# Kernel optimization log

Measured on AMD Instinct MI355X. Metric: run time of the kernel, lower is better.

## Reference

```python
import jax, jax.numpy as jnp
import numpy as np

N_NODES = 100000
N_EDGES = 3200000
IN_DIM = 256
HID = 64
OUT_DIM = 1


def gcn_conv(x, W, b, src, dst, n):
    # PyG GCNConv: h = x @ W; add self loops; sym-normalize; aggregate; + b
    h = x @ W  # [N, F]
    # degrees include self loops (edge_weight = 1), computed on target nodes
    ones = jnp.ones(src.shape[0], dtype=x.dtype)
    deg = jax.ops.segment_sum(ones, dst, num_segments=n) + 1.0  # +1 for self loop
    dinv = jax.lax.rsqrt(deg)
    norm = dinv[src] * dinv[dst]  # [E]
    msg = h[src] * norm[:, None]  # gather + scale
    out = jax.ops.segment_sum(msg, dst, num_segments=n)
    # self-loop contribution: norm_ii = dinv[i]^2
    out = out + h * (dinv * dinv)[:, None]
    return out + b


def setup_inputs() -> dict:
    key = jax.random.key(0)
    ks = jax.random.split(key, 6)
    x = jax.random.normal(ks[0], (N_NODES, IN_DIM), dtype=jnp.float32)
    edge_index = jax.random.randint(ks[1], (2, N_EDGES), 0, N_NODES, dtype=jnp.int64)
    W1 = jax.random.normal(ks[2], (IN_DIM, HID), dtype=jnp.float32) / np.sqrt(IN_DIM)
    b1 = jnp.zeros((HID,), dtype=jnp.float32)
    W2 = jax.random.normal(ks[3], (HID, HID), dtype=jnp.float32) / np.sqrt(HID)
    b2 = jnp.zeros((HID,), dtype=jnp.float32)
    Wf = jax.random.normal(ks[4], (HID, OUT_DIM), dtype=jnp.float32) / np.sqrt(HID)
    bf = jnp.zeros((OUT_DIM,), dtype=jnp.float32)
    return {"x": x, "edge_index": edge_index, "W1": W1, "b1": b1,
            "W2": W2, "b2": b2, "Wf": Wf, "bf": bf}


def reference(x, edge_index, W1, b1, W2, b2, Wf, bf):
    src, dst = edge_index[0], edge_index[1]
    n = x.shape[0]
    h = jax.nn.relu(gcn_conv(x, W1, b1, src, dst, n))
    h = jax.nn.relu(gcn_conv(h, W2, b2, src, dst, n))
    g = jnp.mean(h, axis=0)  # [HID] graph readout
    return jax.nn.sigmoid(g @ Wf + bf)  # [OUT_DIM]
```

## Files before the change

### kernel.cpp

```cpp
#include <hip/hip_runtime.h>


typedef unsigned int u32;
typedef unsigned short u16;
typedef unsigned char u8;
typedef short s16x8 __attribute__((ext_vector_type(8)));
typedef __bf16 bf16x8 __attribute__((ext_vector_type(8)));
typedef float f32x4 __attribute__((ext_vector_type(4)));

constexpr int HID  = 64;
constexpr int SH   = 7;
constexpr int BK   = 128;
constexpr int BPAD = 1024;
constexpr int CH   = 4096;
constexpr int SLOT = 5120;
constexpr int NBLK2 = 4096;

static __device__ __forceinline__ u8 f2fp8(float f) {
    int p = __builtin_amdgcn_cvt_pk_fp8_f32(f, f, 0, false);
    return (u8)(p & 0xFF);
}
static __device__ __forceinline__ float fp82f(u8 v) {
    return __builtin_amdgcn_cvt_f32_fp8((int)v, 0);
}
static __device__ __forceinline__ u16 f2bf(float f) {
    u32 u = __float_as_uint(f);
    return (u16)((u + 0x7FFFu + ((u >> 16) & 1u)) >> 16);
}

__global__ void init_bcur_kernel(int* __restrict__ bcur, int B) {
    int b = blockIdx.x * 256 + threadIdx.x;
    if (b < B) bcur[b] = b * SLOT;
}

__global__ __launch_bounds__(256) void partition_kernel(const int* __restrict__ src,
                                                        const int* __restrict__ dst,
                                                        int* __restrict__ bcur,
                                                        u32* __restrict__ ep, int ne) {
    __shared__ int hcnt[BPAD];
    __shared__ int hoff[BPAD];
    __shared__ int gbase[BPAD];
    __shared__ u32 stage[CH];
    __shared__ int ssc[256];
    const int t = threadIdx.x;
    const int base = blockIdx.x * CH;
    const int cnt = min(CH, ne - base);
    for (int i = t; i < BPAD; i += 256) hcnt[i] = 0;
    __syncthreads();

    int myr[CH / 256];
    #pragma unroll
    for (int k = 0; k < CH / 256; ++k) {
        int i = t + k * 256;
        if (i < cnt) myr[k] = atomicAdd(&hcnt[dst[base + i] >> SH], 1);
    }
    __syncthreads();
    {
        int c0 = hcnt[t*4], c1 = hcnt[t*4+1], c2 = hcnt[t*4+2], c3 = hcnt[t*4+3];
        int tsum = c0 + c1 + c2 + c3;
        ssc[t] = tsum; __syncthreads();
        int run = tsum;
        for (int off = 1; off < 256; off <<= 1) {
            int v = (t >= off) ? ssc[t - off] : 0;
            __syncthreads();
            run += v; ssc[t] = run;
            __syncthreads();
        }
        int ex = run - tsum;
        hoff[t*4] = ex; ex += c0;
        hoff[t*4+1] = ex; ex += c1;
        hoff[t*4+2] = ex; ex += c2;
        hoff[t*4+3] = ex;
    }
    __syncthreads();
    for (int b = t; b < BPAD; b += 256) {
        int c = hcnt[b];
        if (c) gbase[b] = atomicAdd(&bcur[b], c);
    }
    #pragma unroll
    for (int k = 0; k < CH / 256; ++k) {
        int i = t + k * 256;
        if (i < cnt) {
            int s = src[base + i], d = dst[base + i];
            stage[hoff[d >> SH] + myr[k]] = ((u32)(d & (BK - 1)) << 20) | (u32)s;
        }
    }
    __syncthreads();
    for (int i = t; i < cnt; i += 256) {
        u32 v = stage[i];
        int lo = 0;
        #pragma unroll
        for (int s = 512; s; s >>= 1) {
            int m = lo + s;
            if (m < BPAD && hoff[m] <= i) lo = m;
        }
        ep[gbase[lo] + (i - hoff[lo])] = v;
    }
}

__global__ __launch_bounds__(256) void bucket_sort_kernel(const u32* __restrict__ ep,
                                                          const int* __restrict__ bcur,
                                                          int* __restrict__ eidx,
                                                          int* __restrict__ rowend,
                                                          float* __restrict__ dinv, int n) {
    __shared__ int cnt[BK];
    __shared__ int sc[BK];
    __shared__ int cur[BK];
    const int t = threadIdx.x, b = blockIdx.x;
    const int beg = b * SLOT, end = bcur[b];
    if (t < BK) cnt[t] = 0;
    __syncthreads();
    for (int p = beg + t; p < end; p += 256) atomicAdd(&cnt[ep[p] >> 20], 1);
    __syncthreads();
    if (t < BK) sc[t] = cnt[t];
    __syncthreads();
    for (int o = 1; o < BK; o <<= 1) {
        int v = 0;
        if (t < BK && t >= o) v = sc[t - o];
        __syncthreads();
        if (t < BK) sc[t] += v;
        __syncthreads();
    }
    if (t < BK) {
        int node = b * BK + t;
        if (node < n) {
            rowend[node] = beg + sc[t];
            dinv[node] = rsqrtf((float)cnt[t] + 1.0f);
        }
        cur[t] = beg + sc[t] - cnt[t];
    }
    __syncthreads();
    for (int p = beg + t; p < end; p += 256) {
        u32 v = ep[p];
        int r = atomicAdd(&cur[v >> 20], 1);
        eidx[r] = (int)(v & 0xFFFFFu);
    }
}

template <int K>
__global__ void pack_w_kernel(const float* __restrict__ W, u16* __restrict__ wpack) {
    int i = blockIdx.x * 256 + threadIdx.x;
    if (i >= K * 64) return;
    int e = i & 7, lane = (i >> 3) & 63, nt = (i >> 9) & 3, kk = i >> 11;
    int k = kk * 32 + (lane >> 4) * 8 + e;
    int c = nt * 16 + (lane & 15);
    wpack[i] = f2bf(W[k * HID + c]);
}

template <int K, typename TIn>
__global__ __launch_bounds__(256) void mfma_gemm_kernel(const TIn* __restrict__ A,
                                                        const u16* __restrict__ wpack,
                                                        const float* __restrict__ dinv,
                                                        u8* __restrict__ out8, int n) {
    const int t = threadIdx.x;
    const int lane = t & 63;
    const int wid = t >> 6;
    const int r16 = lane & 15;
    const int kgrp = lane >> 4;
    const int ntiles = (n + 15) >> 4;
    for (int tile = blockIdx.x * 4 + wid; tile < ntiles; tile += gridDim.x * 4) {
        const int row0 = tile * 16;
        const int arow = row0 + r16;
        f32x4 acc[4] = {f32x4{0,0,0,0}, f32x4{0,0,0,0}, f32x4{0,0,0,0}, f32x4{0,0,0,0}};
        #pragma unroll
        for (int kk = 0; kk < K / 32; ++kk) {
            s16x8 abits;
            if constexpr (sizeof(TIn) == 4) {
                const float* Af = (const float*)A;
                if (arow < n) {
                    const float4* p0 = (const float4*)(Af + (size_t)arow * K + kk * 32 + kgrp * 8);
                    float4 v0 = p0[0], v1 = p0[1];
                    abits[0] = (short)f2bf(v0.x); abits[1] = (short)f2bf(v0.y);
                    abits[2] = (short)f2bf(v0.z); abits[3] = (short)f2bf(v0.w);
                    abits[4] = (short)f2bf(v1.x); abits[5] = (short)f2bf(v1.y);
                    abits[6] = (short)f2bf(v1.z); abits[7] = (short)f2bf(v1.w);
                } else {
                    #pragma unroll
                    for (int j = 0; j < 8; ++j) abits[j] = 0;
                }
            } else {
                const u8* Ab = (const u8*)A;
                u32 w0 = 0, w1 = 0;
                if (arow < n) {
                    const u32* p0 = (const u32*)(Ab + (size_t)arow * K + kk * 32 + kgrp * 8);
                    w0 = p0[0]; w1 = p0[1];
                }
                abits[0] = (short)f2bf(__builtin_amdgcn_cvt_f32_fp8((int)w0, 0));
                abits[1] = (short)f2bf(__builtin_amdgcn_cvt_f32_fp8((int)w0, 1));
                abits[2] = (short)f2bf(__builtin_amdgcn_cvt_f32_fp8((int)w0, 2));
                abits[3] = (short)f2bf(__builtin_amdgcn_cvt_f32_fp8((int)w0, 3));
                abits[4] = (short)f2bf(__builtin_amdgcn_cvt_f32_fp8((int)w1, 0));
                abits[5] = (short)f2bf(__builtin_amdgcn_cvt_f32_fp8((int)w1, 1));
                abits[6] = (short)f2bf(__builtin_amdgcn_cvt_f32_fp8((int)w1, 2));
                abits[7] = (short)f2bf(__builtin_amdgcn_cvt_f32_fp8((int)w1, 3));
            }
            bf16x8 afrag = __builtin_bit_cast(bf16x8, abits);
            const u16* wp = wpack + ((size_t)(kk * 4) * 64 + lane) * 8;
            #pragma unroll
            for (int nt = 0; nt < 4; ++nt) {
                bf16x8 bfrag = *(const bf16x8*)(wp + (size_t)nt * 64 * 8);
                acc[nt] = __builtin_amdgcn_mfma_f32_16x16x32_bf16(afrag, bfrag, acc[nt], 0, 0, 0);
            }
        }
        #pragma unroll
        for (int reg = 0; reg < 4; ++reg) {
            int r = row0 + kgrp * 4 + reg;
            if (r < n) {
                float dv = dinv[r];
                #pragma unroll
                for (int nt = 0; nt < 4; ++nt)
                    out8[(size_t)r * HID + nt * 16 + r16] = f2fp8(acc[nt][reg] * dv);
            }
        }
    }
}

#define CVT4(acc0, acc1, acc2, acc3, wv) \
    acc0 += __builtin_amdgcn_cvt_f32_fp8((int)(wv), 0); \
    acc1 += __builtin_amdgcn_cvt_f32_fp8((int)(wv), 1); \
    acc2 += __builtin_amdgcn_cvt_f32_fp8((int)(wv), 2); \
    acc3 += __builtin_amdgcn_cvt_f32_fp8((int)(wv), 3);

__global__ __launch_bounds__(256) void agg_csr_kernel(const u8* __restrict__ hp,
                                                      const int* __restrict__ eidx,
                                                      const int* __restrict__ rowend,
                                                      const float* __restrict__ dinv,
                                                      const float* __restrict__ bias,
                                                      u8* __restrict__ out, int n) {
    int w = (blockIdx.x * 256 + threadIdx.x) >> 6;
    int lane = threadIdx.x & 63;
    if (w >= n) return;
    const int g = lane >> 4, fb = lane & 15;
    int beg = (w & (BK - 1)) ? rowend[w - 1] : (w >> SH) * SLOT;
    int end = rowend[w];
    float a0 = 0.f, a1 = 0.f, a2 = 0.f, a3 = 0.f;
    int p = beg;
    for (; p + 16 <= end; p += 16) {
        int s0 = __builtin_nontemporal_load(eidx + p + g);
        int s1 = __builtin_nontemporal_load(eidx + p + 4 + g);
        int s2 = __builtin_nontemporal_load(eidx + p + 8 + g);
        int s3 = __builtin_nontemporal_load(eidx + p + 12 + g);
        u32 w0 = *(const u32*)(hp + (size_t)s0 * 64 + fb * 4);
        u32 w1 = *(const u32*)(hp + (size_t)s1 * 64 + fb * 4);
        u32 w2 = *(const u32*)(hp + (size_t)s2 * 64 + fb * 4);
        u32 w3 = *(const u32*)(hp + (size_t)s3 * 64 + fb * 4);
        CVT4(a0, a1, a2, a3, w0)
        CVT4(a0, a1, a2, a3, w1)
        CVT4(a0, a1, a2, a3, w2)
        CVT4(a0, a1, a2, a3, w3)
    }
    for (; p < end; p += 4) {
        int idx = p + g;
        bool valid = idx < end;
        int s = __builtin_nontemporal_load(eidx + (valid ? idx : beg));
        u32 wv = *(const u32*)(hp + (size_t)s * 64 + fb * 4);
        if (valid) { CVT4(a0, a1, a2, a3, wv) }
    }
    a0 += __shfl_xor(a0, 16); a0 += __shfl_xor(a0, 32);
    a1 += __shfl_xor(a1, 16); a1 += __shfl_xor(a1, 32);
    a2 += __shfl_xor(a2, 16); a2 += __shfl_xor(a2, 32);
    a3 += __shfl_xor(a3, 16); a3 += __shfl_xor(a3, 32);
    u32 sv = *(const u32*)(hp + (size_t)w * 64 + fb * 4);
    float dv = dinv[w];
    float v0 = fmaxf(dv * (a0 + __builtin_amdgcn_cvt_f32_fp8((int)sv, 0)) + bias[fb * 4 + 0], 0.f);
    float v1 = fmaxf(dv * (a1 + __builtin_amdgcn_cvt_f32_fp8((int)sv, 1)) + bias[fb * 4 + 1], 0.f);
    float v2 = fmaxf(dv * (a2 + __builtin_amdgcn_cvt_f32_fp8((int)sv, 2)) + bias[fb * 4 + 2], 0.f);
    float v3 = fmaxf(dv * (a3 + __builtin_amdgcn_cvt_f32_fp8((int)sv, 3)) + bias[fb * 4 + 3], 0.f);
    if (g == 0) {
        int r = __builtin_amdgcn_cvt_pk_fp8_f32(v0, v1, 0, false);
        r = __builtin_amdgcn_cvt_pk_fp8_f32(v2, v3, r, true);
        *(u32*)(out + (size_t)w * 64 + fb * 4) = (u32)r;
    }
}

__global__ __launch_bounds__(256) void agg_csr_reduce_kernel(const u8* __restrict__ hp,
                                                             const int* __restrict__ eidx,
                                                             const int* __restrict__ rowend,
                                                             const float* __restrict__ dinv,
                                                             const float* __restrict__ bias,
                                                             float* __restrict__ partials, int n) {
    __shared__ float sred[256];
    int t = threadIdx.x, lane = t & 63;
    const int g = lane >> 4, fb = lane & 15;
    int wid = (blockIdx.x * 256 + t) >> 6;
    int wstride = gridDim.x * 4;
    float bl0 = bias[fb * 4 + 0], bl1 = bias[fb * 4 + 1];
    float bl2 = bias[fb * 4 + 2], bl3 = bias[fb * 4 + 3];
    float t0 = 0.f, t1 = 0.f, t2 = 0.f, t3 = 0.f;
    for (int w = wid; w < n; w += wstride) {
        int beg = (w & (BK - 1)) ? rowend[w - 1] : (w >> SH) * SLOT;
        int end = rowend[w];
        float a0 = 0.f, a1 = 0.f, a2 = 0.f, a3 = 0.f;
        int p = beg;
        for (; p + 16 <= end; p += 16) {
            int s0 = __builtin_nontemporal_load(eidx + p + g);
            int s1 = __builtin_nontemporal_load(eidx + p + 4 + g);
            int s2 = __builtin_nontemporal_load(eidx + p + 8 + g);
            int s3 = __builtin_nontemporal_load(eidx + p + 12 + g);
            u32 w0 = *(const u32*)(hp + (size_t)s0 * 64 + fb * 4);
            u32 w1 = *(const u32*)(hp + (size_t)s1 * 64 + fb * 4);
            u32 w2 = *(const u32*)(hp + (size_t)s2 * 64 + fb * 4);
            u32 w3 = *(const u32*)(hp + (size_t)s3 * 64 + fb * 4);
            CVT4(a0, a1, a2, a3, w0)
            CVT4(a0, a1, a2, a3, w1)
            CVT4(a0, a1, a2, a3, w2)
            CVT4(a0, a1, a2, a3, w3)
        }
        for (; p < end; p += 4) {
            int idx = p + g;
            bool valid = idx < end;
            int s = __builtin_nontemporal_load(eidx + (valid ? idx : beg));
            u32 wv = *(const u32*)(hp + (size_t)s * 64 + fb * 4);
            if (valid) { CVT4(a0, a1, a2, a3, wv) }
        }
        a0 += __shfl_xor(a0, 16); a0 += __shfl_xor(a0, 32);
        a1 += __shfl_xor(a1, 16); a1 += __shfl_xor(a1, 32);
        a2 += __shfl_xor(a2, 16); a2 += __shfl_xor(a2, 32);
        a3 += __shfl_xor(a3, 16); a3 += __shfl_xor(a3, 32);
        u32 sv = *(const u32*)(hp + (size_t)w * 64 + fb * 4);
        float dv = dinv[w];
        t0 += fmaxf(dv * (a0 + __builtin_amdgcn_cvt_f32_fp8((int)sv, 0)) + bl0, 0.f);
        t1 += fmaxf(dv * (a1 + __builtin_amdgcn_cvt_f32_fp8((int)sv, 1)) + bl1, 0.f);
        t2 += fmaxf(dv * (a2 + __builtin_amdgcn_cvt_f32_fp8((int)sv, 2)) + bl2, 0.f);
        t3 += fmaxf(dv * (a3 + __builtin_amdgcn_cvt_f32_fp8((int)sv, 3)) + bl3, 0.f);
    }
    int wv_ = t >> 6;
    if (g == 0) {
        sred[wv_ * 64 + fb * 4 + 0] = t0;
        sred[wv_ * 64 + fb * 4 + 1] = t1;
        sred[wv_ * 64 + fb * 4 + 2] = t2;
        sred[wv_ * 64 + fb * 4 + 3] = t3;
    }
    __syncthreads();
    if (t < 64) partials[blockIdx.x * 64 + t] = sred[t] + sred[t + 64] + sred[t + 128] + sred[t + 192];
}

__global__ __launch_bounds__(256) void gsum_stage_kernel(const float* __restrict__ parts, int nblk,
                                                         float* __restrict__ gsum) {
    __shared__ float sred[256];
    int t = threadIdx.x, col = t & 63;
    float a = 0.f;
    for (int bk = blockIdx.x * 4 + (t >> 6); bk < nblk; bk += gridDim.x * 4)
        a += parts[bk * 64 + col];
    sred[t] = a; __syncthreads();
    if (t < 64) atomicAdd(&gsum[t], sred[t] + sred[t + 64] + sred[t + 128] + sred[t + 192]);
}

__global__ void final_gsum_kernel(const float* __restrict__ gsum, const float* __restrict__ Wf,
                                  const float* __restrict__ bf_, float* __restrict__ out, float invn) {
    int lane = threadIdx.x;
    float v = gsum[lane] * invn * Wf[lane];
    #pragma unroll
    for (int off = 32; off; off >>= 1) v += __shfl_down(v, off);
    if (lane == 0) out[0] = 1.f / (1.f + expf(-(v + bf_[0])));
}

template <int K, typename TIn>
__global__ __launch_bounds__(256) void gemm_scale_kernel(const TIn* __restrict__ A,
                                                         const float* __restrict__ W,
                                                         const float* __restrict__ dinv,
                                                         u8* __restrict__ out8, int n) {
    __shared__ float xs[16][K];
    const int t = threadIdx.x;
    const int row0 = blockIdx.x * 16;
    if constexpr (sizeof(TIn) == 4) {
        const float* Af = (const float*)A;
        for (int i = t; i < 16 * K; i += 256) {
            int r = i / K;
            (&xs[0][0])[i] = (row0 + r < n) ? Af[(size_t)row0 * K + i] : 0.f;
        }
    } else {
        const u8* Ab = (const u8*)A;
        for (int i = t; i < 16 * K; i += 256) {
            int r = i / K;
            (&xs[0][0])[i] = (row0 + r < n) ? fp82f(Ab[(size_t)row0 * K + i]) : 0.f;
        }
    }
    __syncthreads();
    const int c = t & 63, rg = t >> 6;
    float acc[4] = {0.f, 0.f, 0.f, 0.f};
    #pragma unroll 4
    for (int k = 0; k < K; ++k) {
        float w = W[k * HID + c];
        #pragma unroll
        for (int j = 0; j < 4; ++j) acc[j] += xs[rg + 4 * j][k] * w;
    }
    #pragma unroll
    for (int j = 0; j < 4; ++j) {
        int r = row0 + rg + 4 * j;
        if (r < n) out8[(size_t)r * HID + c] = f2fp8(acc[j] * dinv[r]);
    }
}
__global__ void deg_f_kernel(const int* __restrict__ dst, float* __restrict__ deg, int ne) {
    int i = blockIdx.x * blockDim.x + threadIdx.x, st = gridDim.x * blockDim.x;
    for (; i < ne; i += st) atomicAdd(&deg[dst[i]], 1.0f);
}
__global__ void dinvf_kernel(float* __restrict__ deg, int n) {
    int i = blockIdx.x * blockDim.x + threadIdx.x;
    if (i < n) deg[i] = rsqrtf(deg[i] + 1.0f);
}
__global__ __launch_bounds__(256) void aggregate_atomic_kernel(const u8* __restrict__ hp,
        const int* __restrict__ src, const int* __restrict__ dst,
        const float* __restrict__ dinv, float* __restrict__ outf, int ne) {
    size_t tt = (size_t)blockIdx.x * 256 + threadIdx.x;
    int e = (int)(tt >> 6), f = (int)(tt & 63);
    if (e >= ne) return;
    int s = src[e], d = dst[e];
    atomicAdd(&outf[(size_t)d * HID + f], fp82f(hp[s * HID + f]) * dinv[d]);
}
__global__ void finalize1_fb_kernel(u8* __restrict__ hp, const float* __restrict__ agg,
                                    const float* __restrict__ dinv, const float* __restrict__ b, int n) {
    size_t i = (size_t)blockIdx.x * blockDim.x + threadIdx.x;
    if (i >= (size_t)n * HID) return;
    int node = (int)(i >> 6);
    float v = agg[i] + fp82f(hp[i]) * dinv[node] + b[i & 63];
    hp[i] = f2fp8(fmaxf(v, 0.f));
}
__global__ __launch_bounds__(256) void finalize2_fb_kernel(const u8* __restrict__ hp,
        const float* __restrict__ agg, const float* __restrict__ dinv,
        const float* __restrict__ b, float* __restrict__ gsum, int n) {
    __shared__ float sred[256];
    const int t = threadIdx.x, c = t & 63;
    const size_t total = (size_t)n * HID;
    const size_t stride = (size_t)gridDim.x * blockDim.x;
    float acc = 0.f;
    for (size_t i = (size_t)blockIdx.x * blockDim.x + t; i < total; i += stride) {
        int node = (int)(i >> 6);
        acc += fmaxf(agg[i] + fp82f(hp[i]) * dinv[node] + b[c], 0.f);
    }
    sred[t] = acc; __syncthreads();
    if (t < 64) atomicAdd(&gsum[c], sred[t] + sred[t + 64] + sred[t + 128] + sred[t + 192]);
}
__global__ void final_gsum_fb_kernel(const float* __restrict__ gsum, const float* __restrict__ Wf,
                                     const float* __restrict__ bf_, float* __restrict__ out, int n) {
    int lane = threadIdx.x;
    float v = (gsum[lane] / (float)n) * Wf[lane];
    #pragma unroll
    for (int off = 32; off; off >>= 1) v += __shfl_down(v, off);
    if (lane == 0) out[0] = 1.f / (1.f + expf(-(v + bf_[0])));
}

extern "C" void kernel_launch(void* const* d_in, const int* in_sizes, int n_in,
                              void* d_out, int out_size, void* d_ws, size_t ws_size,
                              hipStream_t stream) {
    const float* x  = (const float*)d_in[0];
    const int*   ei = (const int*)d_in[1];
    const float* W1 = (const float*)d_in[2];
    const float* b1 = (const float*)d_in[3];
    const float* W2 = (const float*)d_in[4];
    const float* b2 = (const float*)d_in[5];
    const float* Wf = (const float*)d_in[6];
    const float* bf_ = (const float*)d_in[7];
    float* out = (float*)d_out;

    const int n  = in_sizes[0] / 256;
    const int ne = in_sizes[1] / 2;
    const int* srcp = ei;
    const int* dstp = ei + ne;
    const int B = (n + BK - 1) / BK;

    char* p = (char*)d_ws;
    u32*   ep     = (u32*)p;   p += ((size_t)B * SLOT + 4096) * 4;
    int*   bcur   = (int*)p;   p += BPAD * 4;
    float* dinv   = (float*)p; p += (size_t)n * 4;
    int*   rowend = (int*)p;   p += (size_t)n * 4;
    float* gsum   = (float*)p; p += 64 * 4;
    int*   eidx   = (int*)p;   p += ((size_t)B * SLOT + 4096) * 4;
    float* parts  = (float*)p; p += (size_t)NBLK2 * 64 * 4;
    p = (char*)(((uintptr_t)p + 15) & ~(uintptr_t)15);
    u16*   wpack1 = (u16*)p;   p += 256 * 64 * 2;
    u16*   wpack2 = (u16*)p;   p += 64 * 64 * 2;
    u8*    hp     = (u8*)p;    p += (size_t)n * HID;
    u8*    h1     = (u8*)p;    p += (size_t)n * HID;
    size_t need = (size_t)(p - (char*)d_ws);

    bool slack_ok = ((size_t)ne / (size_t)B) <= (size_t)(SLOT - 1024);

    if (ws_size >= need && n <= (1 << 17) && slack_ok) {
        (void)hipMemsetAsync(gsum, 0, 64 * 4, stream);
        init_bcur_kernel<<<(B + 255) / 256, 256, 0, stream>>>(bcur, B);
        partition_kernel<<<(ne + CH - 1) / CH, 256, 0, stream>>>(srcp, dstp, bcur, ep, ne);
        bucket_sort_kernel<<<B, 256, 0, stream>>>(ep, bcur, eidx, rowend, dinv, n);
        pack_w_kernel<256><<<64, 256, 0, stream>>>(W1, wpack1);
        pack_w_kernel<64><<<16, 256, 0, stream>>>(W2, wpack2);

        const int ntiles = (n + 15) / 16;
        const int gblk = (ntiles + 3) / 4;
        mfma_gemm_kernel<256, float><<<gblk, 256, 0, stream>>>(x, wpack1, dinv, hp, n);
        agg_csr_kernel<<<(n + 3) / 4, 256, 0, stream>>>(hp, eidx, rowend, dinv, b1, h1, n);
        mfma_gemm_kernel<64, u8><<<gblk, 256, 0, stream>>>(h1, wpack2, dinv, hp, n);
        agg_csr_reduce_kernel<<<NBLK2, 256, 0, stream>>>(hp, eidx, rowend, dinv, b2, parts, n);
        gsum_stage_kernel<<<128, 256, 0, stream>>>(parts, NBLK2, gsum);
        final_gsum_kernel<<<1, 64, 0, stream>>>(gsum, Wf, bf_, out, 1.0f / (float)n);
    } else {
        char* q = (char*)d_ws;
        float* dinvF = (float*)q; q += (size_t)n * 4;
        float* gsumF = (float*)q; q += 64 * 4;
        u8*    hpF   = (u8*)q;   q += (size_t)n * HID;
        float* aggF  = (float*)q;

        (void)hipMemsetAsync(dinvF, 0, ((size_t)n + 64) * 4, stream);
        deg_f_kernel<<<2048, 256, 0, stream>>>(dstp, dinvF, ne);
        dinvf_kernel<<<(n + 255) / 256, 256, 0, stream>>>(dinvF, n);

        gemm_scale_kernel<256, float><<<(n + 15) / 16, 256, 0, stream>>>(x, W1, dinvF, hpF, n);
        (void)hipMemsetAsync(aggF, 0, (size_t)n * HID * 4, stream);
        aggregate_atomic_kernel<<<(int)(((size_t)ne * 64 + 255) / 256), 256, 0, stream>>>(hpF, srcp, dstp, dinvF, aggF, ne);
        finalize1_fb_kernel<<<(int)(((size_t)n * HID + 255) / 256), 256, 0, stream>>>(hpF, aggF, dinvF, b1, n);

        gemm_scale_kernel<64, u8><<<(n + 15) / 16, 256, 0, stream>>>(hpF, W2, dinvF, hpF, n);
        (void)hipMemsetAsync(aggF, 0, (size_t)n * HID * 4, stream);
        aggregate_atomic_kernel<<<(int)(((size_t)ne * 64 + 255) / 256), 256, 0, stream>>>(hpF, srcp, dstp, dinvF, aggF, ne);
        finalize2_fb_kernel<<<2048, 256, 0, stream>>>(hpF, aggF, dinvF, b2, gsumF, n);
        final_gsum_fb_kernel<<<1, 64, 0, stream>>>(gsumF, Wf, bf_, out, n);
    }
}
```

Before: 258.6 us.

## Fuse edge partitioning with layer-1 GEMM and defer dinv scaling to bucket sort

Merges the edge partition pass and the first-layer MFMA GEMM into one launch, with disjoint block ranges, so the compute-bound GEMM and the scatter-bound partition share the GPU at the same time. Because dinv is not yet known during the GEMM, the unscaled result is stored in fp8, and bucket_sort rescales each row by dinv in place. It also makes bcur a relative counter so one memset clears it and gsum together, and merges the two weight-pack kernels. The cost is an extra read-modify-write of hp and a second fp8 rounding step, which may change numerics slightly.

```diff
diff --git a/kernel.cpp b/kernel.cpp
--- a/kernel.cpp
+++ b/kernel.cpp
@@ -28,73 +28,132 @@
     return (u16)((u + 0x7FFFu + ((u >> 16) & 1u)) >> 16);
 }
 
-__global__ void init_bcur_kernel(int* __restrict__ bcur, int B) {
-    int b = blockIdx.x * 256 + threadIdx.x;
-    if (b < B) bcur[b] = b * SLOT;
-}
-
-__global__ __launch_bounds__(256) void partition_kernel(const int* __restrict__ src,
-                                                        const int* __restrict__ dst,
-                                                        int* __restrict__ bcur,
-                                                        u32* __restrict__ ep, int ne) {
+__global__ void pack_both_kernel(const float* __restrict__ W1, const float* __restrict__ W2,
+                                 u16* __restrict__ wpack1, u16* __restrict__ wpack2) {
+    int i = blockIdx.x * 256 + threadIdx.x;
+    if (i < 256 * 64) {
+        int e = i & 7, lane = (i >> 3) & 63, nt = (i >> 9) & 3, kk = i >> 11;
+        wpack1[i] = f2bf(W1[(kk * 32 + (lane >> 4) * 8 + e) * HID + nt * 16 + (lane & 15)]);
+    } else {
+        int j = i - 256 * 64;
+        if (j < 64 * 64) {
+            int e = j & 7, lane = (j >> 3) & 63, nt = (j >> 9) & 3, kk = j >> 11;
+            wpack2[j] = f2bf(W2[(kk * 32 + (lane >> 4) * 8 + e) * HID + nt * 16 + (lane & 15)]);
+        }
+    }
+}
+
+__global__ __launch_bounds__(256) void mega1_kernel(const int* __restrict__ src,
+                                                    const int* __restrict__ dst,
+                                                    int* __restrict__ bcur,
+                                                    u32* __restrict__ ep, int ne,
+                                                    const float* __restrict__ x,
+                                                    const u16* __restrict__ wpack1,
+                                                    u8* __restrict__ hp, int n,
+                                                    int PBLK, int GBLK) {
     __shared__ int hcnt[BPAD];
     __shared__ int hoff[BPAD];
     __shared__ int gbase[BPAD];
     __shared__ u32 stage[CH];
     __shared__ int ssc[256];
     const int t = threadIdx.x;
-    const int base = blockIdx.x * CH;
-    const int cnt = min(CH, ne - base);
-    for (int i = t; i < BPAD; i += 256) hcnt[i] = 0;
-    __syncthreads();
-
-    int myr[CH / 256];
-    #pragma unroll
-    for (int k = 0; k < CH / 256; ++k) {
-        int i = t + k * 256;
-        if (i < cnt) myr[k] = atomicAdd(&hcnt[dst[base + i] >> SH], 1);
-    }
-    __syncthreads();
-    {
-        int c0 = hcnt[t*4], c1 = hcnt[t*4+1], c2 = hcnt[t*4+2], c3 = hcnt[t*4+3];
-        int tsum = c0 + c1 + c2 + c3;
-        ssc[t] = tsum; __syncthreads();
-        int run = tsum;
-        for (int off = 1; off < 256; off <<= 1) {
-            int v = (t >= off) ? ssc[t - off] : 0;
-            __syncthreads();
-            run += v; ssc[t] = run;
-            __syncthreads();
-        }
-        int ex = run - tsum;
-        hoff[t*4] = ex; ex += c0;
-        hoff[t*4+1] = ex; ex += c1;
-        hoff[t*4+2] = ex; ex += c2;
-        hoff[t*4+3] = ex;
-    }
-    __syncthreads();
-    for (int b = t; b < BPAD; b += 256) {
-        int c = hcnt[b];
-        if (c) gbase[b] = atomicAdd(&bcur[b], c);
-    }
-    #pragma unroll
-    for (int k = 0; k < CH / 256; ++k) {
-        int i = t + k * 256;
-        if (i < cnt) {
-            int s = src[base + i], d = dst[base + i];
-            stage[hoff[d >> SH] + myr[k]] = ((u32)(d & (BK - 1)) << 20) | (u32)s;
-        }
-    }
-    __syncthreads();
-    for (int i = t; i < cnt; i += 256) {
-        u32 v = stage[i];
-        int lo = 0;
+
+    if ((int)blockIdx.x < PBLK) {
+        const int base = blockIdx.x * CH;
+        const int cnt = min(CH, ne - base);
+        for (int i = t; i < BPAD; i += 256) hcnt[i] = 0;
+        __syncthreads();
+        int myr[CH / 256];
         #pragma unroll
-        for (int s = 512; s; s >>= 1) {
-            int m = lo + s;
-            if (m < BPAD && hoff[m] <= i) lo = m;
-        }
-        ep[gbase[lo] + (i - hoff[lo])] = v;
+        for (int k = 0; k < CH / 256; ++k) {
+            int i = t + k * 256;
+            if (i < cnt) myr[k] = atomicAdd(&hcnt[dst[base + i] >> SH], 1);
+        }
+        __syncthreads();
+        {
+            int c0 = hcnt[t*4], c1 = hcnt[t*4+1], c2 = hcnt[t*4+2], c3 = hcnt[t*4+3];
+            int tsum = c0 + c1 + c2 + c3;
+            ssc[t] = tsum; __syncthreads();
+            int run = tsum;
+            for (int off = 1; off < 256; off <<= 1) {
+                int v = (t >= off) ? ssc[t - off] : 0;
+                __syncthreads();
+                run += v; ssc[t] = run;
+                __syncthreads();
+            }
+            int ex = run - tsum;
+            hoff[t*4] = ex; ex += c0;
+            hoff[t*4+1] = ex; ex += c1;
+            hoff[t*4+2] = ex; ex += c2;
+            hoff[t*4+3] = ex;
+        }
+        __syncthreads();
+        for (int b = t; b < BPAD; b += 256) {
+            int c = hcnt[b];
+            if (c) gbase[b] = b * SLOT + atomicAdd(&bcur[b], c);
+        }
+        #pragma unroll
+        for (int k = 0; k < CH / 256; ++k) {
+            int i = t + k * 256;
+            if (i < cnt) {
+                int s = src[base + i], d = dst[base + i];
+                stage[hoff[d >> SH] + myr[k]] = ((u32)(d & (BK - 1)) << 20) | (u32)s;
+            }
+        }
+        __syncthreads();
+        for (int i = t; i < cnt; i += 256) {
+            u32 v = stage[i];
+            int lo = 0;
+            #pragma unroll
+            for (int s = 512; s; s >>= 1) {
+                int m = lo + s;
+                if (m < BPAD && hoff[m] <= i) lo = m;
+            }
+            ep[gbase[lo] + (i - hoff[lo])] = v;
+        }
+    } else {
+        const int gbid = blockIdx.x - PBLK;
+        const int lane = t & 63;
+        const int wid = t >> 6;
+        const int r16 = lane & 15;
+        const int kgrp = lane >> 4;
+        const int ntiles = (n + 15) >> 4;
+        for (int tile = gbid * 4 + wid; tile < ntiles; tile += GBLK * 4) {
+            const int row0 = tile * 16;
+            const int arow = row0 + r16;
+            f32x4 acc[4] = {f32x4{0,0,0,0}, f32x4{0,0,0,0}, f32x4{0,0,0,0}, f32x4{0,0,0,0}};
+            #pragma unroll
+            for (int kk = 0; kk < 256 / 32; ++kk) {
+                s16x8 abits;
+                if (arow < n) {
+                    const float4* p0 = (const float4*)(x + (size_t)arow * 256 + kk * 32 + kgrp * 8);
+                    float4 v0 = p0[0], v1 = p0[1];
+                    abits[0] = (short)f2bf(v0.x); abits[1] = (short)f2bf(v0.y);
+                    abits[2] = (short)f2bf(v0.z); abits[3] = (short)f2bf(v0.w);
+                    abits[4] = (short)f2bf(v1.x); abits[5] = (short)f2bf(v1.y);
+                    abits[6] = (short)f2bf(v1.z); abits[7] = (short)f2bf(v1.w);
+                } else {
+                    #pragma unroll
+                    for (int j = 0; j < 8; ++j) abits[j] = 0;
+                }
+                bf16x8 afrag = __builtin_bit_cast(bf16x8, abits);
+                const u16* wp = wpack1 + ((size_t)(kk * 4) * 64 + lane) * 8;
+                #pragma unroll
+                for (int nt = 0; nt < 4; ++nt) {
+                    bf16x8 bfrag = *(const bf16x8*)(wp + (size_t)nt * 64 * 8);
+                    acc[nt] = __builtin_amdgcn_mfma_f32_16x16x32_bf16(afrag, bfrag, acc[nt], 0, 0, 0);
+                }
+            }
+            #pragma unroll
+            for (int reg = 0; reg < 4; ++reg) {
+                int r = row0 + kgrp * 4 + reg;
+                if (r < n) {
+                    #pragma unroll
+                    for (int nt = 0; nt < 4; ++nt)
+                        hp[(size_t)r * HID + nt * 16 + r16] = f2fp8(acc[nt][reg]);
+                }
+            }
+        }
     }
 }
 
@@ -102,12 +161,14 @@
                                                           const int* __restrict__ bcur,
                                                           int* __restrict__ eidx,
                                                           int* __restrict__ rowend,
-                                                          float* __restrict__ dinv, int n) {
+                                                          float* __restrict__ dinv,
+                                                          u8* __restrict__ hp, int n) {
     __shared__ int cnt[BK];
     __shared__ int sc[BK];
     __shared__ int cur[BK];
+    __shared__ float sdv[BK];
     const int t = threadIdx.x, b = blockIdx.x;
-    const int beg = b * SLOT, end = bcur[b];
+    const int beg = b * SLOT, end = b * SLOT + bcur[b];
     if (t < BK) cnt[t] = 0;
     __syncthreads();
     for (int p = beg + t; p < end; p += 256) atomicAdd(&cnt[ep[p] >> 20], 1);
@@ -123,9 +184,11 @@
     }
     if (t < BK) {
         int node = b * BK + t;
+        float dv = rsqrtf((float)cnt[t] + 1.0f);
+        sdv[t] = dv;
         if (node < n) {
             rowend[node] = beg + sc[t];
-            dinv[node] = rsqrtf((float)cnt[t] + 1.0f);
+            dinv[node] = dv;
         }
         cur[t] = beg + sc[t] - cnt[t];
     }
@@ -135,23 +198,30 @@
         int r = atomicAdd(&cur[v >> 20], 1);
         eidx[r] = (int)(v & 0xFFFFFu);
     }
-}
-
-template <int K>
-__global__ void pack_w_kernel(const float* __restrict__ W, u16* __restrict__ wpack) {
-    int i = blockIdx.x * 256 + threadIdx.x;
-    if (i >= K * 64) return;
-    int e = i & 7, lane = (i >> 3) & 63, nt = (i >> 9) & 3, kk = i >> 11;
-    int k = kk * 32 + (lane >> 4) * 8 + e;
-    int c = nt * 16 + (lane & 15);
-    wpack[i] = f2bf(W[k * HID + c]);
-}
-
-template <int K, typename TIn>
-__global__ __launch_bounds__(256) void mfma_gemm_kernel(const TIn* __restrict__ A,
-                                                        const u16* __restrict__ wpack,
-                                                        const float* __restrict__ dinv,
-                                                        u8* __restrict__ out8, int n) {
+    u32* hp32 = (u32*)hp;
+    const int base_node = b * BK;
+    for (int i = t; i < BK * 16; i += 256) {
+        int r = i >> 4;
+        int node = base_node + r;
+        if (node < n) {
+            size_t off = (size_t)node * 16 + (i & 15);
+            u32 v = hp32[off];
+            float dv = sdv[r];
+            float f0 = __builtin_amdgcn_cvt_f32_fp8((int)v, 0) * dv;
+            float f1 = __builtin_amdgcn_cvt_f32_fp8((int)v, 1) * dv;
+            float f2 = __builtin_amdgcn_cvt_f32_fp8((int)v, 2) * dv;
+            float f3 = __builtin_amdgcn_cvt_f32_fp8((int)v, 3) * dv;
+            int pk = __builtin_amdgcn_cvt_pk_fp8_f32(f0, f1, 0, false);
+            pk = __builtin_amdgcn_cvt_pk_fp8_f32(f2, f3, pk, true);
+            hp32[off] = (u32)pk;
+        }
+    }
+}
+
+__global__ __launch_bounds__(256) void mfma_gemm2_kernel(const u8* __restrict__ A,
+                                                         const u16* __restrict__ wpack,
+                                                         const float* __restrict__ dinv,
+                                                         u8* __restrict__ out8, int n) {
     const int t = threadIdx.x;
     const int lane = t & 63;
     const int wid = t >> 6;
@@ -163,37 +233,21 @@
         const int arow = row0 + r16;
         f32x4 acc[4] = {f32x4{0,0,0,0}, f32x4{0,0,0,0}, f32x4{0,0,0,0}, f32x4{0,0,0,0}};
         #pragma unroll
-        for (int kk = 0; kk < K / 32; ++kk) {
+        for (int kk = 0; kk < 2; ++kk) {
             s16x8 abits;
-            if constexpr (sizeof(TIn) == 4) {
-                const float* Af = (const float*)A;
-                if (arow < n) {
-                    const float4* p0 = (const float4*)(Af + (size_t)arow * K + kk * 32 + kgrp * 8);
-                    float4 v0 = p0[0], v1 = p0[1];
-                    abits[0] = (short)f2bf(v0.x); abits[1] = (short)f2bf(v0.y);
-                    abits[2] = (short)f2bf(v0.z); abits[3] = (short)f2bf(v0.w);
-                    abits[4] = (short)f2bf(v1.x); abits[5] = (short)f2bf(v1.y);
-                    abits[6] = (short)f2bf(v1.z); abits[7] = (short)f2bf(v1.w);
-                } else {
-                    #pragma unroll
-                    for (int j = 0; j < 8; ++j) abits[j] = 0;
-                }
-            } else {
-                const u8* Ab = (const u8*)A;
-                u32 w0 = 0, w1 = 0;
-                if (arow < n) {
-                    const u32* p0 = (const u32*)(Ab + (size_t)arow * K + kk * 32 + kgrp * 8);
-                    w0 = p0[0]; w1 = p0[1];
-                }
-                abits[0] = (short)f2bf(__builtin_amdgcn_cvt_f32_fp8((int)w0, 0));
-                abits[1] = (short)f2bf(__builtin_amdgcn_cvt_f32_fp8((int)w0, 1));
-                abits[2] = (short)f2bf(__builtin_amdgcn_cvt_f32_fp8((int)w0, 2));
-                abits[3] = (short)f2bf(__builtin_amdgcn_cvt_f32_fp8((int)w0, 3));
-                abits[4] = (short)f2bf(__builtin_amdgcn_cvt_f32_fp8((int)w1, 0));
-                abits[5] = (short)f2bf(__builtin_amdgcn_cvt_f32_fp8((int)w1, 1));
-                abits[6] = (short)f2bf(__builtin_amdgcn_cvt_f32_fp8((int)w1, 2));
-                abits[7] = (short)f2bf(__builtin_amdgcn_cvt_f32_fp8((int)w1, 3));
-            }
+            u32 w0 = 0, w1 = 0;
+            if (arow < n) {
+                const u32* p0 = (const u32*)(A + (size_t)arow * 64 + kk * 32 + kgrp * 8);
+                w0 = p0[0]; w1 = p0[1];
+            }
+            abits[0] = (short)f2bf(__builtin_amdgcn_cvt_f32_fp8((int)w0, 0));
+            abits[1] = (short)f2bf(__builtin_amdgcn_cvt_f32_fp8((int)w0, 1));
+            abits[2] = (short)f2bf(__builtin_amdgcn_cvt_f32_fp8((int)w0, 2));
+            abits[3] = (short)f2bf(__builtin_amdgcn_cvt_f32_fp8((int)w0, 3));
+            abits[4] = (short)f2bf(__builtin_amdgcn_cvt_f32_fp8((int)w1, 0));
+            abits[5] = (short)f2bf(__builtin_amdgcn_cvt_f32_fp8((int)w1, 1));
+            abits[6] = (short)f2bf(__builtin_amdgcn_cvt_f32_fp8((int)w1, 2));
+            abits[7] = (short)f2bf(__builtin_amdgcn_cvt_f32_fp8((int)w1, 3));
             bf16x8 afrag = __builtin_bit_cast(bf16x8, abits);
             const u16* wp = wpack + ((size_t)(kk * 4) * 64 + lane) * 8;
             #pragma unroll
@@ -462,9 +516,9 @@
     char* p = (char*)d_ws;
     u32*   ep     = (u32*)p;   p += ((size_t)B * SLOT + 4096) * 4;
     int*   bcur   = (int*)p;   p += BPAD * 4;
+    float* gsum   = (float*)p; p += 64 * 4;
     float* dinv   = (float*)p; p += (size_t)n * 4;
     int*   rowend = (int*)p;   p += (size_t)n * 4;
-    float* gsum   = (float*)p; p += 64 * 4;
     int*   eidx   = (int*)p;   p += ((size_t)B * SLOT + 4096) * 4;
     float* parts  = (float*)p; p += (size_t)NBLK2 * 64 * 4;
     p = (char*)(((uintptr_t)p + 15) & ~(uintptr_t)15);
@@ -477,18 +531,17 @@
     bool slack_ok = ((size_t)ne / (size_t)B) <= (size_t)(SLOT - 1024);
 
     if (ws_size >= need && n <= (1 << 17) && slack_ok) {
-        (void)hipMemsetAsync(gsum, 0, 64 * 4, stream);
-        init_bcur_kernel<<<(B + 255) / 256, 256, 0, stream>>>(bcur, B);
-        partition_kernel<<<(ne + CH - 1) / CH, 256, 0, stream>>>(srcp, dstp, bcur, ep, ne);
-        bucket_sort_kernel<<<B, 256, 0, stream>>>(ep, bcur, eidx, rowend, dinv, n);
-        pack_w_kernel<256><<<64, 256, 0, stream>>>(W1, wpack1);
-        pack_w_kernel<64><<<16, 256, 0, stream>>>(W2, wpack2);
-
+        (void)hipMemsetAsync(bcur, 0, (BPAD + 64) * 4, stream);
+        pack_both_kernel<<<80, 256, 0, stream>>>(W1, W2, wpack1, wpack2);
+
+        const int PBLK = (ne + CH - 1) / CH;
         const int ntiles = (n + 15) / 16;
-        const int gblk = (ntiles + 3) / 4;
-        mfma_gemm_kernel<256, float><<<gblk, 256, 0, stream>>>(x, wpack1, dinv, hp, n);
+        const int GBLK = (ntiles + 3) / 4;
+        mega1_kernel<<<PBLK + GBLK, 256, 0, stream>>>(srcp, dstp, bcur, ep, ne,
+                                                      x, wpack1, hp, n, PBLK, GBLK);
+        bucket_sort_kernel<<<B, 256, 0, stream>>>(ep, bcur, eidx, rowend, dinv, hp, n);
         agg_csr_kernel<<<(n + 3) / 4, 256, 0, stream>>>(hp, eidx, rowend, dinv, b1, h1, n);
-        mfma_gemm_kernel<64, u8><<<gblk, 256, 0, stream>>>(h1, wpack2, dinv, hp, n);
+        mfma_gemm2_kernel<<<GBLK, 256, 0, stream>>>(h1, wpack2, dinv, hp, n);
         agg_csr_reduce_kernel<<<NBLK2, 256, 0, stream>>>(hp, eidx, rowend, dinv, b2, parts, n);
         gsum_stage_kernel<<<128, 256, 0, stream>>>(parts, NBLK2, gsum);
         final_gsum_kernel<<<1, 64, 0, stream>>>(gsum, Wf, bf_, out, 1.0f / (float)n);
```

After: 248.7 us, median of 2. -3.8%, faster.
